# Kernel optimization log

Measured on AMD Instinct MI355X. Metric: run time of the kernel, lower is better.

Reference implementation:

```python
import jax, jax.numpy as jnp
import numpy as np

HEADS = 8
DIM_HEAD = 64

def setup_inputs() -> dict:
    key = jax.random.key(0)
    ks = jax.random.split(key, 5)
    B, N, D = 2, 4096, 512  # query_dim = inner_dim = 512
    s = 0.02
    return {
        "x": jax.random.normal(ks[0], (B, N, D), dtype=jnp.float32),
        "Wq": jax.random.normal(ks[1], (D, D), dtype=jnp.float32) * s,
        "Wk": jax.random.normal(ks[2], (D, D), dtype=jnp.float32) * s,
        "Wv": jax.random.normal(ks[3], (D, D), dtype=jnp.float32) * s,
        "Wo": jax.random.normal(ks[4], (D, D), dtype=jnp.float32) * s,
        "bo": jnp.zeros((D,), dtype=jnp.float32),
    }

def reference(x, Wq, Wk, Wv, Wo, bo):
    B, N, D = x.shape
    h, dh = HEADS, DIM_HEAD
    scale = dh ** (-0.5)
    # self-attention: context = x
    q = x @ Wq  # [B, N, h*dh]
    k = x @ Wk
    v = x @ Wv
    # b n (h d) -> b h n d
    q = q.reshape(B, N, h, dh).transpose(0, 2, 1, 3)
    k = k.reshape(B, N, h, dh).transpose(0, 2, 1, 3)
    v = v.reshape(B, N, h, dh).transpose(0, 2, 1, 3)
    sim = jnp.einsum('bhid,bhjd->bhij', q, k) * scale  # full [B,h,N,N] matrix
    attn = jax.nn.softmax(sim, axis=-1)
    out = jnp.einsum('bhij,bhjd->bhid', attn, v)
    out = out.transpose(0, 2, 1, 3).reshape(B, N, h * dh)
    return out @ Wo + bo
```

## Files before the change

### kernel.cpp

```cpp
#include <hip/hip_runtime.h>
#include <hip/hip_bf16.h>
#include <stddef.h>
#include <stdint.h>

typedef __bf16 bf16_t;
typedef bf16_t bf16x8 __attribute__((ext_vector_type(8)));
typedef bf16_t bf16x4 __attribute__((ext_vector_type(4)));
typedef bf16_t bf16x2 __attribute__((ext_vector_type(2)));
typedef float floatx4 __attribute__((ext_vector_type(4)));
typedef float floatx16 __attribute__((ext_vector_type(16)));
typedef int   intx4  __attribute__((ext_vector_type(4)));

#define SEQ    4096
#define DMODEL 512
#define NH     8
#define BATCH  2
#define QSCALE 0.18033688011112042f

__device__ __forceinline__ void ld_lds16(const void* g, void* l) {
  __builtin_amdgcn_global_load_lds(
      (const __attribute__((address_space(1))) unsigned int*)g,
      (__attribute__((address_space(3))) unsigned int*)l, 16, 0, 0);
}

__global__ __launch_bounds__(256) void prep_k(
    const float* __restrict__ x,
    const float* __restrict__ W0, const float* __restrict__ W1,
    const float* __restrict__ W2, const float* __restrict__ W3,
    bf16_t* __restrict__ Wt, bf16_t* __restrict__ xb)
{
  if (blockIdx.z == 4) {
    const floatx4* xf = (const floatx4*)x;
    bf16x4* xo = (bf16x4*)xb;
    int base = (blockIdx.y * 16 + blockIdx.x) * 4096 + threadIdx.x;
    #pragma unroll
    for (int i = 0; i < 16; i++) {
      floatx4 v = xf[base + i * 256];
      xo[base + i * 256] = bf16x4{(bf16_t)v.x, (bf16_t)v.y, (bf16_t)v.z, (bf16_t)v.w};
    }
    return;
  }
  __shared__ float Ws[32][33];
  const float* W = (blockIdx.z == 0) ? W0 : (blockIdx.z == 1) ? W1
                 : (blockIdx.z == 2) ? W2 : W3;
  bf16_t* out = Wt + (size_t)blockIdx.z * DMODEL * DMODEL;
  const int tx = threadIdx.x & 31, ty = threadIdx.x >> 5;
  const int k0 = blockIdx.y * 32, n0 = blockIdx.x * 32;
  #pragma unroll
  for (int i = 0; i < 4; i++) {
    int kk = ty + i * 8;
    Ws[kk][tx] = W[(size_t)(k0 + kk) * DMODEL + n0 + tx];
  }
  __syncthreads();
  #pragma unroll
  for (int i = 0; i < 4; i++) {
    int nn = ty + i * 8;
    out[(size_t)(n0 + nn) * DMODEL + k0 + tx] = (bf16_t)Ws[tx][nn];
  }
}

__global__ __launch_bounds__(256) void qkv_k(
    const bf16_t* __restrict__ xb, const bf16_t* __restrict__ Wt,
    bf16_t* __restrict__ Qw, bf16_t* __restrict__ Ksw, bf16_t* __restrict__ Vsw)
{
  __shared__ __align__(16) char smem[2 * 1536 * 16];
  const int tid  = threadIdx.x;
  const int wave = tid >> 6;
  const int lane = tid & 63;
  const int lh   = lane >> 4, lm = lane & 15;
  const int bm   = blockIdx.x * 128;
  const int mode = blockIdx.y >> 3;
  const int h    = blockIdx.y & 7;
  const bf16_t* Wm = Wt + (size_t)mode * DMODEL * DMODEL;
  const int bn   = h * 64;

  int offA[4], ldsA[4];
  #pragma unroll
  for (int i = 0; i < 4; i++) {
    int S = i * 256 + wave * 64 + lane;
    int r = S >> 3, cc = (S & 7) ^ (r & 7);
    offA[i] = (bm + r) * DMODEL + cc * 8;
    ldsA[i] = (i * 256 + wave * 64) * 16;
  }
  int offB[2], ldsB[2];
  #pragma unroll
  for (int j = 0; j < 2; j++) {
    int S = j * 256 + wave * 64 + lane;
    int n = S >> 3, cc = (S & 7) ^ (n & 7);
    offB[j] = (bn + n) * DMODEL + cc * 8;
    ldsB[j] = (1024 + j * 256 + wave * 64) * 16;
  }

  floatx4 acc[2][4];
  #pragma unroll
  for (int rb = 0; rb < 2; rb++)
    #pragma unroll
    for (int nb = 0; nb < 4; nb++) acc[rb][nb] = floatx4{0.f, 0.f, 0.f, 0.f};

  auto issue = [&](int kt, int buf) {
    char* bp = smem + buf * 1536 * 16;
    #pragma unroll
    for (int i = 0; i < 4; i++) ld_lds16(xb + offA[i] + kt * 64, bp + ldsA[i]);
    #pragma unroll
    for (int j = 0; j < 2; j++) ld_lds16(Wm + offB[j] + kt * 64, bp + ldsB[j]);
  };

  issue(0, 0);
  for (int kt = 0; kt < 8; kt++) {
    __syncthreads();
    if (kt < 7) issue(kt + 1, (kt + 1) & 1);
    const char* bp = smem + (kt & 1) * 1536 * 16;
    #pragma unroll
    for (int ks = 0; ks < 2; ks++) {
      int cc = ks * 4 + lh;
      int rA = wave * 32 + lm;
      bf16x8 a0 = *(const bf16x8*)(bp + (rA * 8 + (cc ^ (rA & 7))) * 16);
      bf16x8 a1 = *(const bf16x8*)(bp + ((rA + 16) * 8 + (cc ^ (rA & 7))) * 16);
      #pragma unroll
      for (int nb = 0; nb < 4; nb++) {
        int n = nb * 16 + lm;
        bf16x8 b = *(const bf16x8*)(bp + (1024 + n * 8 + (cc ^ (n & 7))) * 16);
        acc[0][nb] = __builtin_amdgcn_mfma_f32_16x16x32_bf16(a0, b, acc[0][nb], 0, 0, 0);
        acc[1][nb] = __builtin_amdgcn_mfma_f32_16x16x32_bf16(a1, b, acc[1][nb], 0, 0, 0);
      }
    }
  }

  if (mode == 0) {
    #pragma unroll
    for (int rb = 0; rb < 2; rb++)
      #pragma unroll
      for (int nb = 0; nb < 4; nb++)
        #pragma unroll
        for (int r = 0; r < 4; r++) {
          int row = bm + wave * 32 + rb * 16 + lh * 4 + r;
          Qw[(size_t)row * DMODEL + bn + nb * 16 + lm] =
              (bf16_t)(acc[rb][nb][r] * QSCALE);
        }
  } else if (mode == 1) {
    #pragma unroll
    for (int rb = 0; rb < 2; rb++)
      #pragma unroll
      for (int nb = 0; nb < 4; nb++) {
        int d = nb * 16 + lm;
        #pragma unroll
        for (int r = 0; r < 4; r++) {
          int row = bm + wave * 32 + rb * 16 + lh * 4 + r;
          int bb = row >> 12, tk = row & 4095;
          size_t off = ((size_t)(bb * NH + h) * 64 + (tk >> 6)) * 4096
                     + (size_t)(tk & 63) * 64
                     + ((((d >> 3) ^ (tk & 7)) << 3) | (d & 7));
          Ksw[off] = (bf16_t)acc[rb][nb][r];
        }
      }
  } else {
    __syncthreads();
    bf16_t (*Ts)[136] = (bf16_t(*)[136])smem;
    #pragma unroll
    for (int rb = 0; rb < 2; rb++)
      #pragma unroll
      for (int nb = 0; nb < 4; nb++) {
        int dloc = nb * 16 + lm, tok0 = wave * 32 + rb * 16 + lh * 4;
        bf16x4 v = {(bf16_t)acc[rb][nb][0], (bf16_t)acc[rb][nb][1],
                    (bf16_t)acc[rb][nb][2], (bf16_t)acc[rb][nb][3]};
        *(bf16x4*)&Ts[dloc][tok0] = v;
      }
    __syncthreads();
    const int bb = bm >> 12, tk0 = bm & 4095;
    const size_t hb = (size_t)(bb * NH + h) * 64;
    #pragma unroll
    for (int i = 0; i < 4; i++) {
      int idx = tid + i * 256;
      int d = idx >> 4, c8 = idx & 15;
      bf16x8 val = *(bf16x8*)&Ts[d][c8 * 8];
      int cw = c8 & 7;
      int g = cw >> 1, sub = cw & 1;
      size_t tbase = (hb + (tk0 >> 6) + (c8 >> 3)) * 4096 + (size_t)d * 64;
      bf16x4 v0 = {val[0], val[1], val[2], val[3]};
      bf16x4 v1 = {val[4], val[5], val[6], val[7]};
      *(bf16x4*)&Vsw[tbase + (((2 * g) ^ (d & 7)) << 3) + sub * 4] = v0;
      *(bf16x4*)&Vsw[tbase + (((2 * g + 1) ^ (d & 7)) << 3) + sub * 4] = v1;
    }
  }
}

__global__ __launch_bounds__(256) void out_k(
    const bf16_t* __restrict__ A, const bf16_t* __restrict__ Wt,
    const float* __restrict__ bias, float* __restrict__ out)
{
  __shared__ __align__(16) char smem[2 * 1536 * 16];
  const int tid  = threadIdx.x;
  const int wave = tid >> 6;
  const int lane = tid & 63;
  const int lh   = lane >> 4, lm = lane & 15;
  const int bm   = blockIdx.x * 128;
  const int bn   = blockIdx.y * 64;

  int offA[4], ldsA[4];
  #pragma unroll
  for (int i = 0; i < 4; i++) {
    int S = i * 256 + wave * 64 + lane;
    int r = S >> 3, cc = (S & 7) ^ (r & 7);
    offA[i] = (bm + r) * DMODEL + cc * 8;
    ldsA[i] = (i * 256 + wave * 64) * 16;
  }
  int offB[2], ldsB[2];
  #pragma unroll
  for (int j = 0; j < 2; j++) {
    int S = j * 256 + wave * 64 + lane;
    int n = S >> 3, cc = (S & 7) ^ (n & 7);
    offB[j] = (bn + n) * DMODEL + cc * 8;
    ldsB[j] = (1024 + j * 256 + wave * 64) * 16;
  }

  floatx4 acc[2][4];
  #pragma unroll
  for (int rb = 0; rb < 2; rb++)
    #pragma unroll
    for (int nb = 0; nb < 4; nb++) acc[rb][nb] = floatx4{0.f, 0.f, 0.f, 0.f};

  auto issue = [&](int kt, int buf) {
    char* bp = smem + buf * 1536 * 16;
    #pragma unroll
    for (int i = 0; i < 4; i++) ld_lds16(A + offA[i] + kt * 64, bp + ldsA[i]);
    #pragma unroll
    for (int j = 0; j < 2; j++) ld_lds16(Wt + offB[j] + kt * 64, bp + ldsB[j]);
  };

  issue(0, 0);
  for (int kt = 0; kt < 8; kt++) {
    __syncthreads();
    if (kt < 7) issue(kt + 1, (kt + 1) & 1);
    const char* bp = smem + (kt & 1) * 1536 * 16;
    #pragma unroll
    for (int ks = 0; ks < 2; ks++) {
      int cc = ks * 4 + lh;
      int rA = wave * 32 + lm;
      bf16x8 a0 = *(const bf16x8*)(bp + (rA * 8 + (cc ^ (rA & 7))) * 16);
      bf16x8 a1 = *(const bf16x8*)(bp + ((rA + 16) * 8 + (cc ^ (rA & 7))) * 16);
      #pragma unroll
      for (int nb = 0; nb < 4; nb++) {
        int n = nb * 16 + lm;
        bf16x8 b = *(const bf16x8*)(bp + (1024 + n * 8 + (cc ^ (n & 7))) * 16);
        acc[0][nb] = __builtin_amdgcn_mfma_f32_16x16x32_bf16(a0, b, acc[0][nb], 0, 0, 0);
        acc[1][nb] = __builtin_amdgcn_mfma_f32_16x16x32_bf16(a1, b, acc[1][nb], 0, 0, 0);
      }
    }
  }

  #pragma unroll
  for (int rb = 0; rb < 2; rb++)
    #pragma unroll
    for (int nb = 0; nb < 4; nb++) {
      float bv = bias[bn + nb * 16 + lm];
      #pragma unroll
      for (int r = 0; r < 4; r++) {
        int row = bm + wave * 32 + rb * 16 + lh * 4 + r;
        out[(size_t)row * DMODEL + bn + nb * 16 + lm] = acc[rb][nb][r] + bv;
      }
    }
}

__global__ __launch_bounds__(256, 2) void attn_k(
    const bf16_t* __restrict__ Qw, const bf16_t* __restrict__ Ksw,
    const bf16_t* __restrict__ Vsw, bf16_t* __restrict__ Ow)
{
  __shared__ __align__(16) char smem[2 * 32768];
  const int tid  = threadIdx.x;
  const int wave = tid >> 6;
  const int qh   = wave & 1, kh = wave >> 1;
  const int lane = tid & 63;
  const int hi   = lane >> 5;
  const int lo   = lane & 31;
  const int bh   = blockIdx.y, b = bh >> 3, h = bh & 7;
  const int q0   = blockIdx.x * 128;
  const size_t kvbase = (size_t)bh * 64 * 4096;

  bf16x8 qreg[2][4];
  #pragma unroll
  for (int qc = 0; qc < 2; qc++) {
    int qrow_g = b * SEQ + q0 + qh * 64 + qc * 32 + lo;
    #pragma unroll
    for (int i = 0; i < 4; i++)
      qreg[qc][i] = *(const bf16x8*)&Qw[(size_t)qrow_g * DMODEL + h * 64 + i * 16 + hi * 8];
  }

  floatx16 accO[2][2];
  #pragma unroll
  for (int qc = 0; qc < 2; qc++)
    #pragma unroll
    for (int nbo = 0; nbo < 2; nbo++)
      #pragma unroll
      for (int j = 0; j < 16; j++) accO[qc][nbo][j] = 0.f;
  float ls[2] = {0.f, 0.f};

  auto issue = [&](int s, int buf) {
    char* bp = smem + buf * 32768;
    #pragma unroll
    for (int j = 0; j < 2; j++) {
      const bf16_t* ksrc = Ksw + kvbase + (size_t)(2 * s + j) * 4096;
      const bf16_t* vsrc = Vsw + kvbase + (size_t)(2 * s + j) * 4096;
      #pragma unroll
      for (int half = 0; half < 2; half++) {
        int base = half * 256 + wave * 64;
        ld_lds16(ksrc + (base + lane) * 8, bp + j * 16384 + base * 16);
        ld_lds16(vsrc + (base + lane) * 8, bp + j * 16384 + 8192 + base * 16);
      }
    }
  };

  issue(0, 0);
  for (int s = 0; s < SEQ / 128; s++) {
    __syncthreads();
    if (s < SEQ / 128 - 1) issue(s + 1, (s + 1) & 1);
    const bf16_t* Kb = (const bf16_t*)(smem + (s & 1) * 32768 + kh * 16384);
    const bf16_t* Vb = Kb + 4096;

    floatx16 accS[2][2];
    #pragma unroll
    for (int qc = 0; qc < 2; qc++)
      #pragma unroll
      for (int nb = 0; nb < 2; nb++)
        #pragma unroll
        for (int j = 0; j < 16; j++) accS[qc][nb][j] = 0.f;
    #pragma unroll
    for (int kd = 0; kd < 4; kd++) {
      #pragma unroll
      for (int nb = 0; nb < 2; nb++) {
        int row = nb * 32 + lo;
        bf16x8 ak = *(const bf16x8*)&Kb[row * 64 + (((kd * 2 + hi) ^ (row & 7)) << 3)];
        #pragma unroll
        for (int qc = 0; qc < 2; qc++)
          accS[qc][nb] = __builtin_amdgcn_mfma_f32_32x32x16_bf16(ak, qreg[qc][kd], accS[qc][nb], 0, 0, 0);
      }
    }

    int pkq[2][2][8];
    #pragma unroll
    for (int qc = 0; qc < 2; qc++)
      #pragma unroll
      for (int nb = 0; nb < 2; nb++) {
        float p[16];
        #pragma unroll
        for (int r = 0; r < 16; r++) p[r] = __builtin_amdgcn_exp2f(accS[qc][nb][r]);
        #pragma unroll
        for (int r = 0; r < 16; r += 4)
          ls[qc] += (p[r] + p[r + 1]) + (p[r + 2] + p[r + 3]);
        #pragma unroll
        for (int i = 0; i < 8; i++) {
          bf16x2 t2 = {(bf16_t)p[2 * i], (bf16_t)p[2 * i + 1]};
          pkq[qc][nb][i] = __builtin_bit_cast(int, t2);
        }
      }

    #pragma unroll
    for (int c = 0; c < 4; c++) {
      int nb = c >> 1, c2 = c & 1;
      #pragma unroll
      for (int nbo = 0; nbo < 2; nbo++) {
        int row = nbo * 32 + lo;
        bf16x8 av = *(const bf16x8*)&Vb[row * 64 + (((c * 2 + hi) ^ (row & 7)) << 3)];
        #pragma unroll
        for (int qc = 0; qc < 2; qc++) {
          intx4 pi = {pkq[qc][nb][4 * c2], pkq[qc][nb][4 * c2 + 1],
                      pkq[qc][nb][4 * c2 + 2], pkq[qc][nb][4 * c2 + 3]};
          bf16x8 pf = __builtin_bit_cast(bf16x8, pi);
          accO[qc][nbo] = __builtin_amdgcn_mfma_f32_32x32x16_bf16(av, pf, accO[qc][nbo], 0, 0, 0);
        }
      }
    }
  }

  ls[0] += __shfl_xor(ls[0], 32, 64);
  ls[1] += __shfl_xor(ls[1], 32, 64);
  __syncthreads();
  float* mrg = (float*)smem;
  if (kh == 1) {
    #pragma unroll
    for (int qc = 0; qc < 2; qc++)
      #pragma unroll
      for (int nbo = 0; nbo < 2; nbo++) {
        float* dst = mrg + qh * 4096 + (qc * 2 + nbo) * 1024 + lane * 16;
        #pragma unroll
        for (int g = 0; g < 4; g++) {
          floatx4 v = {accO[qc][nbo][4 * g], accO[qc][nbo][4 * g + 1],
                       accO[qc][nbo][4 * g + 2], accO[qc][nbo][4 * g + 3]};
          *(floatx4*)(dst + 4 * g) = v;
        }
      }
    if (hi == 0) {
      mrg[8192 + qh * 128 + 0 * 64 + lo] = ls[0];
      mrg[8192 + qh * 128 + 1 * 64 + lo] = ls[1];
    }
  }
  __syncthreads();
  if (kh == 0) {
    float linv[2];
    #pragma unroll
    for (int qc = 0; qc < 2; qc++)
      linv[qc] = 1.0f / (ls[qc] + mrg[8192 + qh * 128 + qc * 64 + lo]);
    #pragma unroll
    for (int qc = 0; qc < 2; qc++)
      #pragma unroll
      for (int nbo = 0; nbo < 2; nbo++) {
        const float* src = mrg + qh * 4096 + (qc * 2 + nbo) * 1024 + lane * 16;
        #pragma unroll
        for (int g = 0; g < 4; g++) {
          floatx4 v = *(const floatx4*)(src + 4 * g);
          accO[qc][nbo][4 * g]     += v.x;
          accO[qc][nbo][4 * g + 1] += v.y;
          accO[qc][nbo][4 * g + 2] += v.z;
          accO[qc][nbo][4 * g + 3] += v.w;
        }
      }
    bf16_t* Os = (bf16_t*)(smem + 36864 + qh * 8192);
    #pragma unroll
    for (int qc = 0; qc < 2; qc++)
      #pragma unroll
      for (int nbo = 0; nbo < 2; nbo++)
        #pragma unroll
        for (int g = 0; g < 4; g++) {
          int dbase = g * 8 + 4 * hi + 32 * nbo;
          int qloc = qc * 32 + lo;
          bf16x4 v4 = {(bf16_t)(accO[qc][nbo][4 * g] * linv[qc]),
                       (bf16_t)(accO[qc][nbo][4 * g + 1] * linv[qc]),
                       (bf16_t)(accO[qc][nbo][4 * g + 2] * linv[qc]),
                       (bf16_t)(accO[qc][nbo][4 * g + 3] * linv[qc])};
          *(bf16x4*)&Os[qloc * 64 + (dbase ^ ((qloc & 7) << 3))] = v4;
        }
    #pragma unroll
    for (int i = 0; i < 8; i++) {
      int idx = i * 64 + lane;
      int q = idx >> 3, c8 = idx & 7;
      bf16x8 v = *(const bf16x8*)&Os[q * 64 + ((c8 ^ (q & 7)) << 3)];
      int row_g = b * SEQ + q0 + qh * 64 + q;
      *(bf16x8*)&Ow[(size_t)row_g * DMODEL + h * 64 + c8 * 8] = v;
    }
  }
}

extern "C" void kernel_launch(void* const* d_in, const int* in_sizes, int n_in,
                              void* d_out, int out_size, void* d_ws, size_t ws_size,
                              hipStream_t stream)
{
  const float* x  = (const float*)d_in[0];
  const float* Wq = (const float*)d_in[1];
  const float* Wk = (const float*)d_in[2];
  const float* Wv = (const float*)d_in[3];
  const float* Wo = (const float*)d_in[4];
  const float* bo = (const float*)d_in[5];
  float* out = (float*)d_out;

  const int M = BATCH * SEQ;
  const size_t WT = (size_t)DMODEL * DMODEL;
  const size_t E  = (size_t)M * DMODEL;
  if (ws_size < (4 * WT + 3 * E) * sizeof(bf16_t)) return;

  bf16_t* Wt  = (bf16_t*)d_ws;
  bf16_t* Qw  = Wt + 4 * WT;
  bf16_t* Ksw = Qw + E;
  bf16_t* Vsw = Ksw + E;
  bf16_t* Ow  = Qw;
  bf16_t* xbf = (bf16_t*)d_out;

  prep_k<<<dim3(16, 16, 5), 256, 0, stream>>>(x, Wq, Wk, Wv, Wo, Wt, xbf);

  qkv_k<<<dim3(M / 128, 24), 256, 0, stream>>>(xbf, Wt, Qw, Ksw, Vsw);

  attn_k<<<dim3(SEQ / 128, BATCH * NH), 256, 0, stream>>>(Qw, Ksw, Vsw, Ow);

  out_k<<<dim3(M / 128, DMODEL / 64), 256, 0, stream>>>(Ow, Wt + 3 * WT, bo, out);
}
```

Measured before the change: 177.6 us.

## Split attention work across 8 waves and widen QKV projection tiles

The attention kernel now runs 512-thread blocks, each wave owning 32 query rows instead of 64, with the K/V split kept and a launch bound requesting 4 blocks per CU. This is meant to raise occupancy and shorten per-wave dependency chains, at the cost of twice as many LDS reads of K/V per MFMA and tighter register limits that may cause spills. The QKV projection block now covers 128 output columns (two heads) instead of 64. That halves the grid and reuses each x tile across more MFMAs, but it uses more LDS and accumulator registers per block.

```diff
diff --git a/kernel.cpp b/kernel.cpp
--- a/kernel.cpp
+++ b/kernel.cpp
@@ -63,53 +63,49 @@
     const bf16_t* __restrict__ xb, const bf16_t* __restrict__ Wt,
     bf16_t* __restrict__ Qw, bf16_t* __restrict__ Ksw, bf16_t* __restrict__ Vsw)
 {
-  __shared__ __align__(16) char smem[2 * 1536 * 16];
+  __shared__ __align__(16) char smem[2 * 2048 * 16];
   const int tid  = threadIdx.x;
   const int wave = tid >> 6;
   const int lane = tid & 63;
   const int lh   = lane >> 4, lm = lane & 15;
   const int bm   = blockIdx.x * 128;
-  const int mode = blockIdx.y >> 3;
-  const int h    = blockIdx.y & 7;
+  const int mode = blockIdx.y >> 2;
+  const int hp   = blockIdx.y & 3;
   const bf16_t* Wm = Wt + (size_t)mode * DMODEL * DMODEL;
-  const int bn   = h * 64;
-
-  int offA[4], ldsA[4];
+  const int bn   = hp * 128;
+
+  int offA[4], ldsA[4], offB[4], ldsB[4];
   #pragma unroll
   for (int i = 0; i < 4; i++) {
     int S = i * 256 + wave * 64 + lane;
     int r = S >> 3, cc = (S & 7) ^ (r & 7);
     offA[i] = (bm + r) * DMODEL + cc * 8;
     ldsA[i] = (i * 256 + wave * 64) * 16;
-  }
-  int offB[2], ldsB[2];
-  #pragma unroll
-  for (int j = 0; j < 2; j++) {
-    int S = j * 256 + wave * 64 + lane;
-    int n = S >> 3, cc = (S & 7) ^ (n & 7);
-    offB[j] = (bn + n) * DMODEL + cc * 8;
-    ldsB[j] = (1024 + j * 256 + wave * 64) * 16;
-  }
-
-  floatx4 acc[2][4];
+    int n = S >> 3, cb = (S & 7) ^ (n & 7);
+    offB[i] = (bn + n) * DMODEL + cb * 8;
+    ldsB[i] = (1024 + i * 256 + wave * 64) * 16;
+  }
+
+  floatx4 acc[2][8];
   #pragma unroll
   for (int rb = 0; rb < 2; rb++)
     #pragma unroll
-    for (int nb = 0; nb < 4; nb++) acc[rb][nb] = floatx4{0.f, 0.f, 0.f, 0.f};
+    for (int nb = 0; nb < 8; nb++) acc[rb][nb] = floatx4{0.f, 0.f, 0.f, 0.f};
 
   auto issue = [&](int kt, int buf) {
-    char* bp = smem + buf * 1536 * 16;
-    #pragma unroll
-    for (int i = 0; i < 4; i++) ld_lds16(xb + offA[i] + kt * 64, bp + ldsA[i]);
-    #pragma unroll
-    for (int j = 0; j < 2; j++) ld_lds16(Wm + offB[j] + kt * 64, bp + ldsB[j]);
+    char* bp = smem + buf * 2048 * 16;
+    #pragma unroll
+    for (int i = 0; i < 4; i++) {
+      ld_lds16(xb + offA[i] + kt * 64, bp + ldsA[i]);
+      ld_lds16(Wm + offB[i] + kt * 64, bp + ldsB[i]);
+    }
   };
 
   issue(0, 0);
   for (int kt = 0; kt < 8; kt++) {
     __syncthreads();
     if (kt < 7) issue(kt + 1, (kt + 1) & 1);
-    const char* bp = smem + (kt & 1) * 1536 * 16;
+    const char* bp = smem + (kt & 1) * 2048 * 16;
     #pragma unroll
     for (int ks = 0; ks < 2; ks++) {
       int cc = ks * 4 + lh;
@@ -117,7 +113,7 @@
       bf16x8 a0 = *(const bf16x8*)(bp + (rA * 8 + (cc ^ (rA & 7))) * 16);
       bf16x8 a1 = *(const bf16x8*)(bp + ((rA + 16) * 8 + (cc ^ (rA & 7))) * 16);
       #pragma unroll
-      for (int nb = 0; nb < 4; nb++) {
+      for (int nb = 0; nb < 8; nb++) {
         int n = nb * 16 + lm;
         bf16x8 b = *(const bf16x8*)(bp + (1024 + n * 8 + (cc ^ (n & 7))) * 16);
         acc[0][nb] = __builtin_amdgcn_mfma_f32_16x16x32_bf16(a0, b, acc[0][nb], 0, 0, 0);
@@ -130,7 +126,7 @@
     #pragma unroll
     for (int rb = 0; rb < 2; rb++)
       #pragma unroll
-      for (int nb = 0; nb < 4; nb++)
+      for (int nb = 0; nb < 8; nb++)
         #pragma unroll
         for (int r = 0; r < 4; r++) {
           int row = bm + wave * 32 + rb * 16 + lh * 4 + r;
@@ -141,8 +137,9 @@
     #pragma unroll
     for (int rb = 0; rb < 2; rb++)
       #pragma unroll
-      for (int nb = 0; nb < 4; nb++) {
-        int d = nb * 16 + lm;
+      for (int nb = 0; nb < 8; nb++) {
+        int col = bn + nb * 16 + lm;
+        int h = col >> 6, d = col & 63;
         #pragma unroll
         for (int r = 0; r < 4; r++) {
           int row = bm + wave * 32 + rb * 16 + lh * 4 + r;
@@ -159,7 +156,7 @@
     #pragma unroll
     for (int rb = 0; rb < 2; rb++)
       #pragma unroll
-      for (int nb = 0; nb < 4; nb++) {
+      for (int nb = 0; nb < 8; nb++) {
         int dloc = nb * 16 + lm, tok0 = wave * 32 + rb * 16 + lh * 4;
         bf16x4 v = {(bf16_t)acc[rb][nb][0], (bf16_t)acc[rb][nb][1],
                     (bf16_t)acc[rb][nb][2], (bf16_t)acc[rb][nb][3]};
@@ -167,15 +164,16 @@
       }
     __syncthreads();
     const int bb = bm >> 12, tk0 = bm & 4095;
-    const size_t hb = (size_t)(bb * NH + h) * 64;
-    #pragma unroll
-    for (int i = 0; i < 4; i++) {
+    #pragma unroll
+    for (int i = 0; i < 8; i++) {
       int idx = tid + i * 256;
-      int d = idx >> 4, c8 = idx & 15;
-      bf16x8 val = *(bf16x8*)&Ts[d][c8 * 8];
+      int dl = idx >> 4, c8 = idx & 15;
+      int col = bn + dl, h = col >> 6, d = col & 63;
+      bf16x8 val = *(bf16x8*)&Ts[dl][c8 * 8];
       int cw = c8 & 7;
       int g = cw >> 1, sub = cw & 1;
-      size_t tbase = (hb + (tk0 >> 6) + (c8 >> 3)) * 4096 + (size_t)d * 64;
+      size_t tbase = (((size_t)(bb * NH + h) * 64) + (tk0 >> 6) + (c8 >> 3)) * 4096
+                   + (size_t)d * 64;
       bf16x4 v0 = {val[0], val[1], val[2], val[3]};
       bf16x4 v1 = {val[4], val[5], val[6], val[7]};
       *(bf16x4*)&Vsw[tbase + (((2 * g) ^ (d & 7)) << 3) + sub * 4] = v0;
@@ -261,14 +259,15 @@
     }
 }
 
-__global__ __launch_bounds__(256, 2) void attn_k(
+__global__ __launch_bounds__(512, 4) void attn_k(
     const bf16_t* __restrict__ Qw, const bf16_t* __restrict__ Ksw,
     const bf16_t* __restrict__ Vsw, bf16_t* __restrict__ Ow)
 {
   __shared__ __align__(16) char smem[2 * 32768];
   const int tid  = threadIdx.x;
   const int wave = tid >> 6;
-  const int qh   = wave & 1, kh = wave >> 1;
+  const int qh   = wave >> 1;
+  const int kh   = wave & 1;
   const int lane = tid & 63;
   const int hi   = lane >> 5;
   const int lo   = lane & 31;
@@ -276,37 +275,29 @@
   const int q0   = blockIdx.x * 128;
   const size_t kvbase = (size_t)bh * 64 * 4096;
 
-  bf16x8 qreg[2][4];
-  #pragma unroll
-  for (int qc = 0; qc < 2; qc++) {
-    int qrow_g = b * SEQ + q0 + qh * 64 + qc * 32 + lo;
-    #pragma unroll
-    for (int i = 0; i < 4; i++)
-      qreg[qc][i] = *(const bf16x8*)&Qw[(size_t)qrow_g * DMODEL + h * 64 + i * 16 + hi * 8];
-  }
-
-  floatx16 accO[2][2];
-  #pragma unroll
-  for (int qc = 0; qc < 2; qc++)
-    #pragma unroll
-    for (int nbo = 0; nbo < 2; nbo++)
-      #pragma unroll
-      for (int j = 0; j < 16; j++) accO[qc][nbo][j] = 0.f;
-  float ls[2] = {0.f, 0.f};
+  const int qrow_g = b * SEQ + q0 + qh * 32 + lo;
+  bf16x8 qreg[4];
+  #pragma unroll
+  for (int i = 0; i < 4; i++)
+    qreg[i] = *(const bf16x8*)&Qw[(size_t)qrow_g * DMODEL + h * 64 + i * 16 + hi * 8];
+
+  floatx16 accO[2];
+  #pragma unroll
+  for (int nbo = 0; nbo < 2; nbo++)
+    #pragma unroll
+    for (int j = 0; j < 16; j++) accO[nbo][j] = 0.f;
+  float ls = 0.f;
 
   auto issue = [&](int s, int buf) {
     char* bp = smem + buf * 32768;
-    #pragma unroll
-    for (int j = 0; j < 2; j++) {
-      const bf16_t* ksrc = Ksw + kvbase + (size_t)(2 * s + j) * 4096;
-      const bf16_t* vsrc = Vsw + kvbase + (size_t)(2 * s + j) * 4096;
-      #pragma unroll
-      for (int half = 0; half < 2; half++) {
-        int base = half * 256 + wave * 64;
-        ld_lds16(ksrc + (base + lane) * 8, bp + j * 16384 + base * 16);
-        ld_lds16(vsrc + (base + lane) * 8, bp + j * 16384 + 8192 + base * 16);
-      }
-    }
+    const bf16_t* k0 = Ksw + kvbase + (size_t)(2 * s) * 4096;
+    const bf16_t* v0 = Vsw + kvbase + (size_t)(2 * s) * 4096;
+    const bf16_t* k1 = k0 + 4096;
+    const bf16_t* v1 = v0 + 4096;
+    ld_lds16(k0 + tid * 8, bp + tid * 16);
+    ld_lds16(v0 + tid * 8, bp + 8192 + tid * 16);
+    ld_lds16(k1 + tid * 8, bp + 16384 + tid * 16);
+    ld_lds16(v1 + tid * 8, bp + 24576 + tid * 16);
   };
 
   issue(0, 0);
@@ -316,124 +307,100 @@
     const bf16_t* Kb = (const bf16_t*)(smem + (s & 1) * 32768 + kh * 16384);
     const bf16_t* Vb = Kb + 4096;
 
-    floatx16 accS[2][2];
-    #pragma unroll
-    for (int qc = 0; qc < 2; qc++)
-      #pragma unroll
-      for (int nb = 0; nb < 2; nb++)
-        #pragma unroll
-        for (int j = 0; j < 16; j++) accS[qc][nb][j] = 0.f;
+    floatx16 accS[2];
+    #pragma unroll
+    for (int nb = 0; nb < 2; nb++)
+      #pragma unroll
+      for (int j = 0; j < 16; j++) accS[nb][j] = 0.f;
     #pragma unroll
     for (int kd = 0; kd < 4; kd++) {
       #pragma unroll
       for (int nb = 0; nb < 2; nb++) {
         int row = nb * 32 + lo;
         bf16x8 ak = *(const bf16x8*)&Kb[row * 64 + (((kd * 2 + hi) ^ (row & 7)) << 3)];
-        #pragma unroll
-        for (int qc = 0; qc < 2; qc++)
-          accS[qc][nb] = __builtin_amdgcn_mfma_f32_32x32x16_bf16(ak, qreg[qc][kd], accS[qc][nb], 0, 0, 0);
-      }
-    }
-
-    int pkq[2][2][8];
-    #pragma unroll
-    for (int qc = 0; qc < 2; qc++)
-      #pragma unroll
-      for (int nb = 0; nb < 2; nb++) {
-        float p[16];
-        #pragma unroll
-        for (int r = 0; r < 16; r++) p[r] = __builtin_amdgcn_exp2f(accS[qc][nb][r]);
-        #pragma unroll
-        for (int r = 0; r < 16; r += 4)
-          ls[qc] += (p[r] + p[r + 1]) + (p[r + 2] + p[r + 3]);
-        #pragma unroll
-        for (int i = 0; i < 8; i++) {
-          bf16x2 t2 = {(bf16_t)p[2 * i], (bf16_t)p[2 * i + 1]};
-          pkq[qc][nb][i] = __builtin_bit_cast(int, t2);
-        }
-      }
+        accS[nb] = __builtin_amdgcn_mfma_f32_32x32x16_bf16(ak, qreg[kd], accS[nb], 0, 0, 0);
+      }
+    }
+
+    int pk[2][8];
+    #pragma unroll
+    for (int nb = 0; nb < 2; nb++) {
+      float p[16];
+      #pragma unroll
+      for (int r = 0; r < 16; r++) p[r] = __builtin_amdgcn_exp2f(accS[nb][r]);
+      #pragma unroll
+      for (int r = 0; r < 16; r += 4)
+        ls += (p[r] + p[r + 1]) + (p[r + 2] + p[r + 3]);
+      #pragma unroll
+      for (int i = 0; i < 8; i++) {
+        bf16x2 t2 = {(bf16_t)p[2 * i], (bf16_t)p[2 * i + 1]};
+        pk[nb][i] = __builtin_bit_cast(int, t2);
+      }
+    }
 
     #pragma unroll
     for (int c = 0; c < 4; c++) {
-      int nb = c >> 1, c2 = c & 1;
+      intx4 pi = {pk[c >> 1][4 * (c & 1)],     pk[c >> 1][4 * (c & 1) + 1],
+                  pk[c >> 1][4 * (c & 1) + 2], pk[c >> 1][4 * (c & 1) + 3]};
+      bf16x8 pf = __builtin_bit_cast(bf16x8, pi);
       #pragma unroll
       for (int nbo = 0; nbo < 2; nbo++) {
         int row = nbo * 32 + lo;
         bf16x8 av = *(const bf16x8*)&Vb[row * 64 + (((c * 2 + hi) ^ (row & 7)) << 3)];
-        #pragma unroll
-        for (int qc = 0; qc < 2; qc++) {
-          intx4 pi = {pkq[qc][nb][4 * c2], pkq[qc][nb][4 * c2 + 1],
-                      pkq[qc][nb][4 * c2 + 2], pkq[qc][nb][4 * c2 + 3]};
-          bf16x8 pf = __builtin_bit_cast(bf16x8, pi);
-          accO[qc][nbo] = __builtin_amdgcn_mfma_f32_32x32x16_bf16(av, pf, accO[qc][nbo], 0, 0, 0);
-        }
-      }
-    }
-  }
-
-  ls[0] += __shfl_xor(ls[0], 32, 64);
-  ls[1] += __shfl_xor(ls[1], 32, 64);
+        accO[nbo] = __builtin_amdgcn_mfma_f32_32x32x16_bf16(av, pf, accO[nbo], 0, 0, 0);
+      }
+    }
+  }
+
+  ls += __shfl_xor(ls, 32, 64);
   __syncthreads();
   float* mrg = (float*)smem;
   if (kh == 1) {
     #pragma unroll
-    for (int qc = 0; qc < 2; qc++)
-      #pragma unroll
-      for (int nbo = 0; nbo < 2; nbo++) {
-        float* dst = mrg + qh * 4096 + (qc * 2 + nbo) * 1024 + lane * 16;
-        #pragma unroll
-        for (int g = 0; g < 4; g++) {
-          floatx4 v = {accO[qc][nbo][4 * g], accO[qc][nbo][4 * g + 1],
-                       accO[qc][nbo][4 * g + 2], accO[qc][nbo][4 * g + 3]};
-          *(floatx4*)(dst + 4 * g) = v;
-        }
-      }
-    if (hi == 0) {
-      mrg[8192 + qh * 128 + 0 * 64 + lo] = ls[0];
-      mrg[8192 + qh * 128 + 1 * 64 + lo] = ls[1];
-    }
+    for (int nbo = 0; nbo < 2; nbo++) {
+      float* dst = mrg + qh * 2048 + nbo * 1024 + lane * 16;
+      #pragma unroll
+      for (int g = 0; g < 4; g++) {
+        floatx4 v = {accO[nbo][4 * g], accO[nbo][4 * g + 1],
+                     accO[nbo][4 * g + 2], accO[nbo][4 * g + 3]};
+        *(floatx4*)(dst + 4 * g) = v;
+      }
+    }
+    if (hi == 0) mrg[8192 + qh * 32 + lo] = ls;
   }
   __syncthreads();
   if (kh == 0) {
-    float linv[2];
-    #pragma unroll
-    for (int qc = 0; qc < 2; qc++)
-      linv[qc] = 1.0f / (ls[qc] + mrg[8192 + qh * 128 + qc * 64 + lo]);
-    #pragma unroll
-    for (int qc = 0; qc < 2; qc++)
-      #pragma unroll
-      for (int nbo = 0; nbo < 2; nbo++) {
-        const float* src = mrg + qh * 4096 + (qc * 2 + nbo) * 1024 + lane * 16;
-        #pragma unroll
-        for (int g = 0; g < 4; g++) {
-          floatx4 v = *(const floatx4*)(src + 4 * g);
-          accO[qc][nbo][4 * g]     += v.x;
-          accO[qc][nbo][4 * g + 1] += v.y;
-          accO[qc][nbo][4 * g + 2] += v.z;
-          accO[qc][nbo][4 * g + 3] += v.w;
-        }
-      }
-    bf16_t* Os = (bf16_t*)(smem + 36864 + qh * 8192);
-    #pragma unroll
-    for (int qc = 0; qc < 2; qc++)
-      #pragma unroll
-      for (int nbo = 0; nbo < 2; nbo++)
-        #pragma unroll
-        for (int g = 0; g < 4; g++) {
-          int dbase = g * 8 + 4 * hi + 32 * nbo;
-          int qloc = qc * 32 + lo;
-          bf16x4 v4 = {(bf16_t)(accO[qc][nbo][4 * g] * linv[qc]),
-                       (bf16_t)(accO[qc][nbo][4 * g + 1] * linv[qc]),
-                       (bf16_t)(accO[qc][nbo][4 * g + 2] * linv[qc]),
-                       (bf16_t)(accO[qc][nbo][4 * g + 3] * linv[qc])};
-          *(bf16x4*)&Os[qloc * 64 + (dbase ^ ((qloc & 7) << 3))] = v4;
-        }
-    #pragma unroll
-    for (int i = 0; i < 8; i++) {
+    float linv = 1.0f / (ls + mrg[8192 + qh * 32 + lo]);
+    #pragma unroll
+    for (int nbo = 0; nbo < 2; nbo++) {
+      const float* src = mrg + qh * 2048 + nbo * 1024 + lane * 16;
+      #pragma unroll
+      for (int g = 0; g < 4; g++) {
+        floatx4 v = *(const floatx4*)(src + 4 * g);
+        accO[nbo][4 * g]     += v.x;
+        accO[nbo][4 * g + 1] += v.y;
+        accO[nbo][4 * g + 2] += v.z;
+        accO[nbo][4 * g + 3] += v.w;
+      }
+    }
+    bf16_t* Os = (bf16_t*)(smem + 36864 + qh * 4096);
+    #pragma unroll
+    for (int nbo = 0; nbo < 2; nbo++)
+      #pragma unroll
+      for (int g = 0; g < 4; g++) {
+        int dbase = g * 8 + 4 * hi + 32 * nbo;
+        bf16x4 v4 = {(bf16_t)(accO[nbo][4 * g] * linv),
+                     (bf16_t)(accO[nbo][4 * g + 1] * linv),
+                     (bf16_t)(accO[nbo][4 * g + 2] * linv),
+                     (bf16_t)(accO[nbo][4 * g + 3] * linv)};
+        *(bf16x4*)&Os[lo * 64 + (dbase ^ ((lo & 7) << 3))] = v4;
+      }
+    #pragma unroll
+    for (int i = 0; i < 4; i++) {
       int idx = i * 64 + lane;
       int q = idx >> 3, c8 = idx & 7;
       bf16x8 v = *(const bf16x8*)&Os[q * 64 + ((c8 ^ (q & 7)) << 3)];
-      int row_g = b * SEQ + q0 + qh * 64 + q;
+      int row_g = b * SEQ + q0 + qh * 32 + q;
       *(bf16x8*)&Ow[(size_t)row_g * DMODEL + h * 64 + c8 * 8] = v;
     }
   }
@@ -465,9 +432,9 @@
 
   prep_k<<<dim3(16, 16, 5), 256, 0, stream>>>(x, Wq, Wk, Wv, Wo, Wt, xbf);
 
-  qkv_k<<<dim3(M / 128, 24), 256, 0, stream>>>(xbf, Wt, Qw, Ksw, Vsw);
-
-  attn_k<<<dim3(SEQ / 128, BATCH * NH), 256, 0, stream>>>(Qw, Ksw, Vsw, Ow);
+  qkv_k<<<dim3(M / 128, 12), 256, 0, stream>>>(xbf, Wt, Qw, Ksw, Vsw);
+
+  attn_k<<<dim3(SEQ / 128, BATCH * NH), 512, 0, stream>>>(Qw, Ksw, Vsw, Ow);
 
   out_k<<<dim3(M / 128, DMODEL / 64), 256, 0, stream>>>(Ow, Wt + 3 * WT, bo, out);
 }
```

Result: no change. 174.6 us (-1.7%).
